# Performance work log

Measured on AMD Instinct MI355X. Metric: run time of the kernel, lower is better.

Reference implementation:

```python
import jax, jax.numpy as jnp
import numpy as np

R, N_X, N_MONTE = 8192, 32, 64


def setup_inputs() -> dict:
    key = jax.random.key(0)
    ks = jax.random.split(key, 6)
    # SPD per-step Hessian blocks (recog_x_prec_tilde is PSD by construction in the model)
    B = jax.random.normal(ks[0], (R, N_X, N_X), dtype=jnp.float32)
    x_hessian_diags = jnp.einsum('rij,rkj->rik', B, B) / N_X + jnp.eye(N_X, dtype=jnp.float32)
    x_grads = jax.random.normal(ks[1], (R, 1, N_X), dtype=jnp.float32)
    x_trans_mat = 0.5 * jnp.eye(N_X, dtype=jnp.float32) + 0.1 * jax.random.normal(ks[2], (N_X, N_X), dtype=jnp.float32)
    A = jax.random.normal(ks[3], (N_X, N_X), dtype=jnp.float32)
    x_trans_prec = A @ A.T / N_X + jnp.eye(N_X, dtype=jnp.float32)
    Bi = jax.random.normal(ks[4], (N_X, N_X), dtype=jnp.float32)
    x_init_prec = Bi @ Bi.T / N_X + jnp.eye(N_X, dtype=jnp.float32)
    epsx = jax.random.normal(ks[5], (R, N_MONTE, N_X), dtype=jnp.float32)
    return dict(x_hessian_diags=x_hessian_diags, x_grads=x_grads, x_trans_mat=x_trans_mat,
                x_trans_prec=x_trans_prec, x_init_prec=x_init_prec, epsx=epsx)


def _cholesky_update(x_hessian_diags, x_grads, x_trans_mat, x_trans_prec, x_init_prec, epsx):
    Rn, n_monte, n_x = epsx.shape
    solve = jax.scipy.linalg.solve_triangular
    MtP = x_trans_mat @ x_trans_prec          # [n_x, n_x]
    MtPMt = MtP @ x_trans_mat.T               # [n_x, n_x]
    # last step has no transition term (m=0), matching ms = [1,...,1,0]
    ms = jnp.concatenate([jnp.ones((Rn - 1,), jnp.float32), jnp.zeros((1,), jnp.float32)])

    def fwd(carry, elem):
        P, C, u = carry                       # predicted prec, off-diag chol, u
        H, g, m = elem
        L = jnp.linalg.cholesky(P + H + m * MtPMt)          # [n_x, n_x] lower
        u = solve(L, (g - u @ C.T).T, lower=True).T         # [1, n_x]
        C = solve(L, -MtP, lower=True).T                    # [n_x, n_x]
        P = x_trans_prec - C @ C.T
        return (P, C, u), (L, C, u)

    z = jnp.zeros((n_x, n_x), jnp.float32)
    init = (x_init_prec, z, jnp.zeros((1, n_x), jnp.float32))
    _, (Ls, Cs, us) = jax.lax.scan(fwd, init, (x_hessian_diags, x_grads, ms))

    gs = jnp.concatenate([us, epsx], axis=1)  # [R, 1+n_monte, n_x]

    def bwd(vw, elem):
        L, C, g = elem
        vw = solve(L.T, (g - vw @ C).T, lower=False).T      # [1+n_monte, n_x]
        return vw, vw

    _, vws = jax.lax.scan(bwd, jnp.zeros((n_monte + 1, n_x), jnp.float32),
                          (Ls, Cs, gs), reverse=True)
    vs, ws = vws[:, :1], vws[:, 1:]           # posterior mean part, sample part
    return Ls, Cs, vs, ws


def reference(x_hessian_diags, x_grads, x_trans_mat, x_trans_prec, x_init_prec, epsx):
    _, _, vs, ws = _cholesky_update(x_hessian_diags, x_grads, x_trans_mat,
                                    x_trans_prec, x_init_prec, epsx)
    # x_tilde = vs_tilde + ws_tilde as used downstream in _compute_eta_loss_2
    return vs + ws                            # [R, n_monte, n_x]
```

## Files before the change

### kernel.cpp

```cpp
#include <hip/hip_runtime.h>
#include <stdint.h>

#define RTOT 8192
#define BFWD 4
#define WFWD 12
#define BBWD 16
#define WBWD 16
#define LSTR 36

typedef unsigned short u16;
typedef __attribute__((ext_vector_type(4))) float f32x4;
typedef __attribute__((ext_vector_type(8))) unsigned short u16x8;

__device__ __forceinline__ float bf2f(u16 u) { return __uint_as_float(((uint32_t)u) << 16); }
__device__ __forceinline__ float rdlane(float v, int l) {
  return __int_as_float(__builtin_amdgcn_readlane(__float_as_int(v), l));
}

__device__ __forceinline__ void load8(const void* p, size_t off, bool bf, float* o) {
  if (bf) {
    u16x8 v = *(const u16x8*)((const u16*)p + off);
    #pragma unroll
    for (int e = 0; e < 8; ++e) o[e] = bf2f(v[e]);
  } else {
    f32x4 a = *(const f32x4*)((const float*)p + off);
    f32x4 b = *(const f32x4*)((const float*)p + off + 4);
    o[0]=a[0]; o[1]=a[1]; o[2]=a[2]; o[3]=a[3];
    o[4]=b[0]; o[5]=b[1]; o[6]=b[2]; o[7]=b[3];
  }
}
__device__ __forceinline__ float load1(const void* p, size_t off, bool bf) {
  return bf ? bf2f(((const u16*)p)[off]) : ((const float*)p)[off];
}

__global__ void detect_kernel(const void* Wptr, int* flag) {
  if (threadIdx.x == 0) {
    const u16* w = (const u16*)Wptr;
    int ok = 1;
    const int pi[4] = {0, 0, 1, 2};
    const int pj[4] = {1, 2, 2, 3};
    #pragma unroll
    for (int p = 0; p < 4; ++p)
      ok &= (w[pi[p]*32 + pj[p]] == w[pj[p]*32 + pi[p]]) ? 1 : 0;
    *flag = ok;
  }
}

__global__ __launch_bounds__(64, 2) void fwd_kernel(
    const void* __restrict__ Hg, const void* __restrict__ Gg,
    const void* __restrict__ Mg, const void* __restrict__ Wg,
    const void* __restrict__ Ig, int s0, const int* __restrict__ flag,
    float* __restrict__ gLinv, float* __restrict__ gCt, float* __restrict__ gU)
{
  __shared__ __align__(16) float ldsCt[32*LSTR];
  __shared__ __align__(16) float ldsLinv[32*LSTR];
  __shared__ float ldsU[32];

  const bool bf = (*flag != 0);
  const int lane = threadIdx.x & 63;
  const int il = lane & 31;
  const bool lo = (lane < 32);
  const int hoff = (lane >> 5) * 16;

  float wrow[32], mrow[32];
  #pragma unroll
  for (int c = 0; c < 4; ++c) {
    float wt[8], mt[8];
    load8(Wg, il*32 + c*8, bf, wt);
    load8(Mg, il*32 + c*8, bf, mt);
    #pragma unroll
    for (int e = 0; e < 8; ++e) {
      wrow[c*8+e] = wt[e]; mrow[c*8+e] = mt[e];
      ldsCt[il*LSTR + c*8+e] = mt[e];
    }
  }
  __syncthreads();

  #pragma unroll 4
  for (int m = 0; m < 32; ++m) {
    float acc = 0.0f;
    #pragma unroll
    for (int c = 0; c < 8; ++c) {
      f32x4 q = *(const f32x4*)&ldsCt[m*LSTR + c*4];
      acc = fmaf(q[0], wrow[c*4+0], acc); acc = fmaf(q[1], wrow[c*4+1], acc);
      acc = fmaf(q[2], wrow[c*4+2], acc); acc = fmaf(q[3], wrow[c*4+3], acc);
    }
    ldsLinv[m*LSTR + il] = acc;
  }
  __syncthreads();
  #pragma unroll 4
  for (int m = 0; m < 32; ++m) {
    float acc = 0.0f;
    #pragma unroll
    for (int c = 0; c < 8; ++c) {
      f32x4 q = *(const f32x4*)&ldsLinv[m*LSTR + c*4];
      acc = fmaf(q[0], mrow[c*4+0], acc); acc = fmaf(q[1], mrow[c*4+1], acc);
      acc = fmaf(q[2], mrow[c*4+2], acc); acc = fmaf(q[3], mrow[c*4+3], acc);
    }
    ldsCt[m*LSTR + il] = acc;
  }
  __syncthreads();

  float mtpcol[32];
  #pragma unroll
  for (int t = 0; t < 32; ++t) mtpcol[t] = ldsLinv[t*LSTR + il];
  float k0h[16];
  #pragma unroll
  for (int c = 0; c < 16; ++c) {
    float a = wrow[c]      + ldsCt[il*LSTR + c];
    float b = wrow[c + 16] + ldsCt[il*LSTR + 16 + c];
    k0h[c] = lo ? a : b;
  }
  __syncthreads();

  #pragma unroll
  for (int k = 0; k < 32; ++k) ldsCt[il*LSTR + k] = 0.0f;
  if (lo) ldsU[il] = 0.0f;
  __syncthreads();

  const int r0 = s0 + blockIdx.x * BFWD;
  const int rw0 = (r0 >= WFWD) ? (r0 - WFWD) : 0;
  const int rend = r0 + BFWD;

  float hcur[16];
  #pragma unroll
  for (int c = 0; c < 2; ++c)
    load8(Hg, (size_t)rw0*1024 + il*32 + hoff + c*8, bf, &hcur[c*8]);
  float gv = load1(Gg, (size_t)rw0*32 + il, bf);

  for (int r = rw0; r < rend; ++r) {
    int rn = (r + 1 < RTOT) ? (r + 1) : r;
    float hnext[16];
    #pragma unroll
    for (int c = 0; c < 2; ++c)
      load8(Hg, (size_t)rn*1024 + il*32 + hoff + c*8, bf, &hnext[c*8]);
    float gvn = load1(Gg, (size_t)rn*32 + il, bf);

    float sv[16];
    if (r == 0) {
      #pragma unroll
      for (int c = 0; c < 2; ++c) {
        float it[8], wt[8];
        load8(Ig, il*32 + hoff + c*8, bf, it);
        load8(Wg, il*32 + hoff + c*8, bf, wt);
        #pragma unroll
        for (int e = 0; e < 8; ++e)
          sv[c*8+e] = hcur[c*8+e] + it[e] + (k0h[c*8+e] - wt[e]);
      }
    } else if (r == RTOT - 1) {
      #pragma unroll
      for (int c = 0; c < 2; ++c) {
        float wt[8];
        load8(Wg, il*32 + hoff + c*8, bf, wt);
        #pragma unroll
        for (int e = 0; e < 8; ++e) sv[c*8+e] = hcur[c*8+e] + wt[e];
      }
    } else {
      #pragma unroll
      for (int k = 0; k < 16; ++k) sv[k] = hcur[k] + k0h[k];
    }

    float y = gv;
    #pragma unroll 4
    for (int m = 0; m < 32; ++m) {
      float cm = ldsCt[m*LSTR + il];
      y = fmaf(ldsU[m], cm, y);
      #pragma unroll
      for (int c = 0; c < 4; ++c) {
        f32x4 q = *(const f32x4*)&ldsCt[m*LSTR + hoff + c*4];
        sv[c*4+0] = fmaf(-cm, q[0], sv[c*4+0]);
        sv[c*4+1] = fmaf(-cm, q[1], sv[c*4+1]);
        sv[c*4+2] = fmaf(-cm, q[2], sv[c*4+2]);
        sv[c*4+3] = fmaf(-cm, q[3], sv[c*4+3]);
      }
    }

    float v[32];
    #pragma unroll
    for (int c = 0; c < 16; ++c) {
      float o = __shfl_xor(sv[c], 32, 64);
      v[c]      = lo ? sv[c] : mtpcol[c];
      v[c + 16] = lo ? o     : mtpcol[c + 16];
    }

    float un = 0.0f;
    float yr = y;
    if (r < r0) {
      #pragma unroll
      for (int j = 0; j < 32; ++j) {
        float dj = fmaxf(rdlane(v[j], j), 1e-12f);
        float rs = __builtin_amdgcn_rsqf(dj);
        float a = v[j] * rs;
        v[j] = a;
        float uj = rdlane(yr, j) * rs;
        yr = fmaf(-a, uj, yr);
        if (il == j) un = uj;
        #pragma unroll
        for (int k = j + 1; k < 32; ++k) {
          float bk = rdlane(v[j], k);
          v[k] = fmaf(-a, bk, v[k]);
        }
      }
    } else {
      float w[32];
      #pragma unroll
      for (int i = 0; i < 32; ++i) w[i] = (lo && il == i) ? 1.0f : 0.0f;
      #pragma unroll
      for (int j = 0; j < 32; ++j) {
        float dj = fmaxf(rdlane(v[j], j), 1e-12f);
        float rs = __builtin_amdgcn_rsqf(dj);
        float a = v[j] * rs;
        v[j] = a;
        float b = w[j] * rs;
        w[j] = b;
        float uj = rdlane(yr, j) * rs;
        yr = fmaf(-a, uj, yr);
        if (il == j) un = uj;
        #pragma unroll
        for (int k = j + 1; k < 32; ++k) {
          float bk = rdlane(v[j], k);
          v[k] = fmaf(-a, bk, v[k]);
          w[k] = fmaf(-b, bk, w[k]);
        }
      }
      if (lo) {
        #pragma unroll
        for (int i = 0; i < 32; ++i) ldsLinv[i*LSTR + il] = w[i];
      }
    }

    if (!lo) {
      #pragma unroll
      for (int m = 0; m < 32; ++m) ldsCt[m*LSTR + il] = v[m];
    } else {
      ldsU[il] = un;
    }

    if (r >= r0) {
      __syncthreads();
      size_t ro = (size_t)(r - s0);
      #pragma unroll
      for (int c = 0; c < 4; ++c) {
        int f = lane*16 + c*4;
        int mm = f >> 5, kk = f & 31;
        *(f32x4*)&gLinv[ro*1024 + f] = *(const f32x4*)&ldsLinv[mm*LSTR + kk];
        *(f32x4*)&gCt [ro*1024 + f] = *(const f32x4*)&ldsCt [mm*LSTR + kk];
      }
      if (lo) gU[ro*32 + il] = un;
    }

    #pragma unroll
    for (int e = 0; e < 16; ++e) hcur[e] = hnext[e];
    gv = gvn;
  }
}

__global__ __launch_bounds__(256, 2) void mid_kernel(
    const void* __restrict__ Eg, const int* __restrict__ flag,
    float* __restrict__ gLinv, float* __restrict__ gCt,
    float* __restrict__ gU, float* __restrict__ gY2, int s0)
{
  __shared__ __align__(16) float Li[32*LSTR];
  __shared__ __align__(16) float Ct_[32*LSTR];
  __shared__ float Ut[32];

  const bool bf = (*flag != 0);
  const int t = threadIdx.x;
  const size_t ro = blockIdx.x;
  const size_t r = (size_t)s0 + ro;

  {
    int mm = t >> 3, kk = (t & 7) * 4;
    *(f32x4*)&Li[mm*LSTR + kk]  = *(const f32x4*)&gLinv[ro*1024 + t*4];
    *(f32x4*)&Ct_[mm*LSTR + kk] = *(const f32x4*)&gCt [ro*1024 + t*4];
    if (t < 32) Ut[t] = gU[ro*32 + t];
  }
  __syncthreads();

  {
    int s = t >> 2, oct = t & 3;
    float er[32];
    #pragma unroll
    for (int c = 0; c < 4; ++c) load8(Eg, (r*64 + (size_t)s)*32 + c*8, bf, &er[c*8]);
    float a0=0,a1=0,a2=0,a3=0,a4=0,a5=0,a6=0,a7=0;
    #pragma unroll 4
    for (int k = 0; k < 32; ++k) {
      f32x4 b  = *(const f32x4*)&Li[k*LSTR + oct*8];
      f32x4 b2 = *(const f32x4*)&Li[k*LSTR + oct*8 + 4];
      float ek = er[k];
      a0=fmaf(ek,b[0],a0);  a1=fmaf(ek,b[1],a1);
      a2=fmaf(ek,b[2],a2);  a3=fmaf(ek,b[3],a3);
      a4=fmaf(ek,b2[0],a4); a5=fmaf(ek,b2[1],a5);
      a6=fmaf(ek,b2[2],a6); a7=fmaf(ek,b2[3],a7);
    }
    float* dst = (s < 32) ? (gLinv + ro*1024 + (size_t)s*32)
                          : (gY2  + ro*1024 + (size_t)(s-32)*32);
    f32x4 va = {a0,a1,a2,a3}, vb = {a4,a5,a6,a7};
    *(f32x4*)&dst[oct*8] = va;
    *(f32x4*)&dst[oct*8 + 4] = vb;
  }

  {
    int m = t >> 3, jo = t & 7;
    float d0=0,d1=0,d2=0,d3=0;
    #pragma unroll 4
    for (int k = 0; k < 32; ++k) {
      float cv = Ct_[k*LSTR + m];
      f32x4 b = *(const f32x4*)&Li[k*LSTR + jo*4];
      d0=fmaf(cv,b[0],d0); d1=fmaf(cv,b[1],d1);
      d2=fmaf(cv,b[2],d2); d3=fmaf(cv,b[3],d3);
    }
    f32x4 dv = {d0,d1,d2,d3};
    *(f32x4*)&gCt[ro*1024 + (size_t)m*32 + jo*4] = dv;
  }

  if (t < 32) {
    float a = 0.0f;
    #pragma unroll
    for (int k = 0; k < 32; ++k) a = fmaf(Ut[k], Li[k*LSTR + t], a);
    gU[ro*32 + t] = a;
  }
}

__global__ __launch_bounds__(256, 2) void bwd_kernel(
    const float* __restrict__ gD,
    const float* __restrict__ gY1,
    const float* __restrict__ gY2,
    const float* __restrict__ gY0,
    float* __restrict__ outg, int s0)
{
  __shared__ __align__(16) float vw[65*LSTR];
  __shared__ __align__(16) float Dl[2][32*LSTR];
  __shared__ __align__(16) float v0buf[2][32];

  const int t = threadIdx.x;
  const int pr = t >> 3;
  const int o  = t & 7;
  const int rowA = pr, rowB = pr + 32;
  const bool x64 = (t < 8);
  const int r0 = s0 + blockIdx.x * BBWD;
  int re = r0 + BBWD - 1 + WBWD; if (re > RTOT - 1) re = RTOT - 1;

  for (int i = t; i < 65*LSTR; i += 256) vw[i] = 0.0f;

  #define YPTR(RO_, S_) \
    ((S_) == 0  ? (gY0 + (size_t)(RO_)*32) : \
     (S_) <= 32 ? (gY1 + (size_t)(RO_)*1024 + (size_t)((S_)-1)*32) \
                : (gY2 + (size_t)(RO_)*1024 + (size_t)((S_)-33)*32))

  f32x4 z = {0,0,0,0};
  const int reo = re - s0;
  f32x4 pD = *(const f32x4*)&gD[(size_t)reo*1024 + t*4];
  f32x4 yA, yB, yC = z;
  yA = *(const f32x4*)&(YPTR(reo, rowA))[o*4];
  yB = *(const f32x4*)&(YPTR(reo, rowB))[o*4];
  if (x64) yC = *(const f32x4*)&(YPTR(reo, 64))[o*4];
  *(f32x4*)&Dl[re & 1][pr*LSTR + o*4] = pD;
  if (re > r0) pD = *(const f32x4*)&gD[(size_t)(reo-1)*1024 + t*4];
  __syncthreads();

  for (int r = re; r >= r0; --r) {
    const int cur = r & 1;
    const int ro = r - s0;

    if (r > r0) *(f32x4*)&Dl[cur ^ 1][pr*LSTR + o*4] = pD;
    f32x4 nyA = z, nyB = z, nyC = z;
    if (r - 1 > r0) pD = *(const f32x4*)&gD[(size_t)(ro-2)*1024 + t*4];
    if (r > r0) {
      nyA = *(const f32x4*)&(YPTR(ro - 1, rowA))[o*4];
      nyB = *(const f32x4*)&(YPTR(ro - 1, rowB))[o*4];
      if (x64) nyC = *(const f32x4*)&(YPTR(ro - 1, 64))[o*4];
    }

    float vrA[32], vrB[32];
    #pragma unroll
    for (int c = 0; c < 8; ++c) {
      f32x4 qa = *(const f32x4*)&vw[rowA*LSTR + c*4];
      f32x4 qb = *(const f32x4*)&vw[rowB*LSTR + c*4];
      vrA[c*4+0]=qa[0]; vrA[c*4+1]=qa[1]; vrA[c*4+2]=qa[2]; vrA[c*4+3]=qa[3];
      vrB[c*4+0]=qb[0]; vrB[c*4+1]=qb[1]; vrB[c*4+2]=qb[2]; vrB[c*4+3]=qb[3];
    }

    float a0=yA[0],a1=yA[1],a2=yA[2],a3=yA[3];
    float b0=yB[0],b1=yB[1],b2=yB[2],b3=yB[3];
    #pragma unroll 4
    for (int k = 0; k < 32; ++k) {
      f32x4 d = *(const f32x4*)&Dl[cur][k*LSTR + o*4];
      float xa = vrA[k], xb = vrB[k];
      a0=fmaf(xa,d[0],a0); a1=fmaf(xa,d[1],a1);
      a2=fmaf(xa,d[2],a2); a3=fmaf(xa,d[3],a3);
      b0=fmaf(xb,d[0],b0); b1=fmaf(xb,d[1],b1);
      b2=fmaf(xb,d[2],b2); b3=fmaf(xb,d[3],b3);
    }
    f32x4 va = {a0,a1,a2,a3}, vb = {b0,b1,b2,b3};
    *(f32x4*)&vw[rowA*LSTR + o*4] = va;
    *(f32x4*)&vw[rowB*LSTR + o*4] = vb;

    float c0=0,c1=0,c2=0,c3=0;
    if (x64) {
      *(f32x4*)&v0buf[cur][o*4] = va;
      float vrC[32];
      #pragma unroll
      for (int c = 0; c < 8; ++c) {
        f32x4 q = *(const f32x4*)&vw[64*LSTR + c*4];
        vrC[c*4+0]=q[0]; vrC[c*4+1]=q[1]; vrC[c*4+2]=q[2]; vrC[c*4+3]=q[3];
      }
      c0=yC[0]; c1=yC[1]; c2=yC[2]; c3=yC[3];
      #pragma unroll 4
      for (int k = 0; k < 32; ++k) {
        f32x4 d = *(const f32x4*)&Dl[cur][k*LSTR + o*4];
        float xc = vrC[k];
        c0=fmaf(xc,d[0],c0); c1=fmaf(xc,d[1],c1);
        c2=fmaf(xc,d[2],c2); c3=fmaf(xc,d[3],c3);
      }
      f32x4 vc = {c0,c1,c2,c3};
      *(f32x4*)&vw[64*LSTR + o*4] = vc;
    }

    __syncthreads();

    if (r < r0 + BBWD) {
      f32x4 v0 = *(const f32x4*)&v0buf[cur][o*4];
      if (pr >= 1) {
        float* dst = outg + ((size_t)r*64 + (size_t)(pr-1))*32 + o*4;
        f32x4 oo = {a0+v0[0], a1+v0[1], a2+v0[2], a3+v0[3]};
        *(f32x4*)dst = oo;
      }
      {
        float* dst = outg + ((size_t)r*64 + (size_t)(pr+31))*32 + o*4;
        f32x4 oo = {b0+v0[0], b1+v0[1], b2+v0[2], b3+v0[3]};
        *(f32x4*)dst = oo;
      }
      if (x64) {
        float* dst = outg + ((size_t)r*64 + 63)*32 + o*4;
        f32x4 oo = {c0+v0[0], c1+v0[1], c2+v0[2], c3+v0[3]};
        *(f32x4*)dst = oo;
      }
    }

    yA = nyA; yB = nyB;
    if (x64) yC = nyC;
  }
  #undef YPTR
}

extern "C" void kernel_launch(void* const* d_in, const int* in_sizes, int n_in,
                              void* d_out, int out_size, void* d_ws, size_t ws_size,
                              hipStream_t stream) {
  (void)in_sizes; (void)n_in; (void)out_size;
  const void* H = d_in[0];
  const void* G = d_in[1];
  const void* M = d_in[2];
  const void* W = d_in[3];
  const void* I = d_in[4];
  const void* E = d_in[5];
  float* out = (float*)d_out;

  int* flag = (int*)d_ws;
  float* ws0 = (float*)((char*)d_ws + 256);
  size_t avail = (ws_size > 256) ? (ws_size - 256) : 0;

  int nseg = 64;
  for (int cand = 1; cand <= 64; cand <<= 1) {
    size_t nrext = (size_t)(RTOT / cand) + WBWD;
    if (nrext * 12416 <= avail) { nseg = cand; break; }
  }
  const int segrows = RTOT / nseg;
  const size_t nrext_max = (size_t)segrows + WBWD;

  float* gLinv = ws0;
  float* gCt  = ws0 + nrext_max * 1024;
  float* gU   = ws0 + nrext_max * 2048;
  float* gY2  = ws0 + nrext_max * 2080;

  detect_kernel<<<1, 64, 0, stream>>>(W, flag);

  for (int s = 0; s < nseg; ++s) {
    int s0 = s * segrows;
    int s1ext = s0 + segrows + WBWD; if (s1ext > RTOT) s1ext = RTOT;
    int nr = s1ext - s0;
    int nfb = (nr + BFWD - 1) / BFWD;
    fwd_kernel<<<nfb, 64, 0, stream>>>(H, G, M, W, I, s0, flag, gLinv, gCt, gU);
    mid_kernel<<<nr, 256, 0, stream>>>(E, flag, gLinv, gCt, gU, gY2, s0);
    bwd_kernel<<<segrows / BBWD, 256, 0, stream>>>(gCt, gLinv, gY2, gU, out, s0);
  }
}
```

Before: 416.3 us.

## Fold mean term into sample rows and run backward scan in one wavefront

The mid kernel now adds the posterior-mean contribution (u·Linv) directly into every sample row's injected term. The mean row no longer has to be propagated separately, so the backward scan only tracks 64 rows. The backward kernel is rewritten as a single 64-lane wavefront that keeps each row's state in registers and broadcasts the D matrix via readlane. This removes LDS traffic and __syncthreads from the serial recurrence, and the backward block size is halved to raise the number of blocks. The cost is 32×32 readlane-fed FMAs per lane per step, plus more redundant warm-up steps relative to useful rows.

```diff
diff --git a/kernel.cpp b/kernel.cpp
--- a/kernel.cpp
+++ b/kernel.cpp
@@ -4,7 +4,7 @@
 #define RTOT 8192
 #define BFWD 4
 #define WFWD 12
-#define BBWD 16
+#define BBWD 8
 #define WBWD 16
 #define LSTR 36
 
@@ -258,11 +258,12 @@
 __global__ __launch_bounds__(256, 2) void mid_kernel(
     const void* __restrict__ Eg, const int* __restrict__ flag,
     float* __restrict__ gLinv, float* __restrict__ gCt,
-    float* __restrict__ gU, float* __restrict__ gY2, int s0)
+    const float* __restrict__ gU, float* __restrict__ gY2, int s0)
 {
   __shared__ __align__(16) float Li[32*LSTR];
   __shared__ __align__(16) float Ct_[32*LSTR];
   __shared__ float Ut[32];
+  __shared__ float Y0l[32];
 
   const bool bf = (*flag != 0);
   const int t = threadIdx.x;
@@ -274,6 +275,14 @@
     *(f32x4*)&Li[mm*LSTR + kk]  = *(const f32x4*)&gLinv[ro*1024 + t*4];
     *(f32x4*)&Ct_[mm*LSTR + kk] = *(const f32x4*)&gCt [ro*1024 + t*4];
     if (t < 32) Ut[t] = gU[ro*32 + t];
+  }
+  __syncthreads();
+
+  if (t < 32) {
+    float a = 0.0f;
+    #pragma unroll
+    for (int k = 0; k < 32; ++k) a = fmaf(Ut[k], Li[k*LSTR + t], a);
+    Y0l[t] = a;
   }
   __syncthreads();
 
@@ -293,9 +302,12 @@
       a4=fmaf(ek,b2[0],a4); a5=fmaf(ek,b2[1],a5);
       a6=fmaf(ek,b2[2],a6); a7=fmaf(ek,b2[3],a7);
     }
+    f32x4 y0a = *(const f32x4*)&Y0l[oct*8];
+    f32x4 y0b = *(const f32x4*)&Y0l[oct*8 + 4];
     float* dst = (s < 32) ? (gLinv + ro*1024 + (size_t)s*32)
                           : (gY2  + ro*1024 + (size_t)(s-32)*32);
-    f32x4 va = {a0,a1,a2,a3}, vb = {a4,a5,a6,a7};
+    f32x4 va = {a0+y0a[0], a1+y0a[1], a2+y0a[2], a3+y0a[3]};
+    f32x4 vb = {a4+y0b[0], a5+y0b[1], a6+y0b[2], a7+y0b[3]};
     *(f32x4*)&dst[oct*8] = va;
     *(f32x4*)&dst[oct*8 + 4] = vb;
   }
@@ -313,135 +325,80 @@
     f32x4 dv = {d0,d1,d2,d3};
     *(f32x4*)&gCt[ro*1024 + (size_t)m*32 + jo*4] = dv;
   }
-
-  if (t < 32) {
-    float a = 0.0f;
-    #pragma unroll
-    for (int k = 0; k < 32; ++k) a = fmaf(Ut[k], Li[k*LSTR + t], a);
-    gU[ro*32 + t] = a;
-  }
-}
-
-__global__ __launch_bounds__(256, 2) void bwd_kernel(
+}
+
+__global__ __launch_bounds__(64, 1) void bwd_kernel(
     const float* __restrict__ gD,
     const float* __restrict__ gY1,
     const float* __restrict__ gY2,
-    const float* __restrict__ gY0,
     float* __restrict__ outg, int s0)
 {
-  __shared__ __align__(16) float vw[65*LSTR];
-  __shared__ __align__(16) float Dl[2][32*LSTR];
-  __shared__ __align__(16) float v0buf[2][32];
-
-  const int t = threadIdx.x;
-  const int pr = t >> 3;
-  const int o  = t & 7;
-  const int rowA = pr, rowB = pr + 32;
-  const bool x64 = (t < 8);
+  const int l = threadIdx.x & 63;
+  const int lr = l & 31;
+  const int dco = (l >> 5) * 16;
   const int r0 = s0 + blockIdx.x * BBWD;
   int re = r0 + BBWD - 1 + WBWD; if (re > RTOT - 1) re = RTOT - 1;
 
-  for (int i = t; i < 65*LSTR; i += 256) vw[i] = 0.0f;
-
-  #define YPTR(RO_, S_) \
-    ((S_) == 0  ? (gY0 + (size_t)(RO_)*32) : \
-     (S_) <= 32 ? (gY1 + (size_t)(RO_)*1024 + (size_t)((S_)-1)*32) \
-                : (gY2 + (size_t)(RO_)*1024 + (size_t)((S_)-33)*32))
-
-  f32x4 z = {0,0,0,0};
+  const float* Yb = (l < 32) ? gY1 : gY2;
+
+  float vwr[32];
+  #pragma unroll
+  for (int k = 0; k < 32; ++k) vwr[k] = 0.0f;
+
   const int reo = re - s0;
-  f32x4 pD = *(const f32x4*)&gD[(size_t)reo*1024 + t*4];
-  f32x4 yA, yB, yC = z;
-  yA = *(const f32x4*)&(YPTR(reo, rowA))[o*4];
-  yB = *(const f32x4*)&(YPTR(reo, rowB))[o*4];
-  if (x64) yC = *(const f32x4*)&(YPTR(reo, 64))[o*4];
-  *(f32x4*)&Dl[re & 1][pr*LSTR + o*4] = pD;
-  if (re > r0) pD = *(const f32x4*)&gD[(size_t)(reo-1)*1024 + t*4];
-  __syncthreads();
+  f32x4 Dc[4], Yc[8];
+  #pragma unroll
+  for (int c = 0; c < 4; ++c)
+    Dc[c] = *(const f32x4*)&gD[(size_t)reo*1024 + (size_t)lr*32 + dco + c*4];
+  #pragma unroll
+  for (int c = 0; c < 8; ++c)
+    Yc[c] = *(const f32x4*)&Yb[(size_t)reo*1024 + (size_t)lr*32 + c*4];
 
   for (int r = re; r >= r0; --r) {
-    const int cur = r & 1;
     const int ro = r - s0;
 
-    if (r > r0) *(f32x4*)&Dl[cur ^ 1][pr*LSTR + o*4] = pD;
-    f32x4 nyA = z, nyB = z, nyC = z;
-    if (r - 1 > r0) pD = *(const f32x4*)&gD[(size_t)(ro-2)*1024 + t*4];
+    f32x4 Dn[4], Yn[8];
     if (r > r0) {
-      nyA = *(const f32x4*)&(YPTR(ro - 1, rowA))[o*4];
-      nyB = *(const f32x4*)&(YPTR(ro - 1, rowB))[o*4];
-      if (x64) nyC = *(const f32x4*)&(YPTR(ro - 1, 64))[o*4];
-    }
-
-    float vrA[32], vrB[32];
-    #pragma unroll
-    for (int c = 0; c < 8; ++c) {
-      f32x4 qa = *(const f32x4*)&vw[rowA*LSTR + c*4];
-      f32x4 qb = *(const f32x4*)&vw[rowB*LSTR + c*4];
-      vrA[c*4+0]=qa[0]; vrA[c*4+1]=qa[1]; vrA[c*4+2]=qa[2]; vrA[c*4+3]=qa[3];
-      vrB[c*4+0]=qb[0]; vrB[c*4+1]=qb[1]; vrB[c*4+2]=qb[2]; vrB[c*4+3]=qb[3];
-    }
-
-    float a0=yA[0],a1=yA[1],a2=yA[2],a3=yA[3];
-    float b0=yB[0],b1=yB[1],b2=yB[2],b3=yB[3];
-    #pragma unroll 4
-    for (int k = 0; k < 32; ++k) {
-      f32x4 d = *(const f32x4*)&Dl[cur][k*LSTR + o*4];
-      float xa = vrA[k], xb = vrB[k];
-      a0=fmaf(xa,d[0],a0); a1=fmaf(xa,d[1],a1);
-      a2=fmaf(xa,d[2],a2); a3=fmaf(xa,d[3],a3);
-      b0=fmaf(xb,d[0],b0); b1=fmaf(xb,d[1],b1);
-      b2=fmaf(xb,d[2],b2); b3=fmaf(xb,d[3],b3);
-    }
-    f32x4 va = {a0,a1,a2,a3}, vb = {b0,b1,b2,b3};
-    *(f32x4*)&vw[rowA*LSTR + o*4] = va;
-    *(f32x4*)&vw[rowB*LSTR + o*4] = vb;
-
-    float c0=0,c1=0,c2=0,c3=0;
-    if (x64) {
-      *(f32x4*)&v0buf[cur][o*4] = va;
-      float vrC[32];
+      #pragma unroll
+      for (int c = 0; c < 4; ++c)
+        Dn[c] = *(const f32x4*)&gD[(size_t)(ro-1)*1024 + (size_t)lr*32 + dco + c*4];
+      #pragma unroll
+      for (int c = 0; c < 8; ++c)
+        Yn[c] = *(const f32x4*)&Yb[(size_t)(ro-1)*1024 + (size_t)lr*32 + c*4];
+    }
+
+    float nv[32];
+    #pragma unroll
+    for (int j = 0; j < 32; ++j) {
+      float acc = Yc[j >> 2][j & 3];
+      const int cidx = j & 15;
+      const int sadd = (j >> 4) << 5;
+      #pragma unroll
+      for (int k = 0; k < 32; ++k) {
+        float dkj = rdlane(Dc[cidx >> 2][cidx & 3], k + sadd);
+        acc = fmaf(vwr[k], dkj, acc);
+      }
+      nv[j] = acc;
+    }
+
+    if (r < r0 + BBWD) {
+      float* dst = outg + ((size_t)r * 64 + (size_t)l) * 32;
       #pragma unroll
       for (int c = 0; c < 8; ++c) {
-        f32x4 q = *(const f32x4*)&vw[64*LSTR + c*4];
-        vrC[c*4+0]=q[0]; vrC[c*4+1]=q[1]; vrC[c*4+2]=q[2]; vrC[c*4+3]=q[3];
-      }
-      c0=yC[0]; c1=yC[1]; c2=yC[2]; c3=yC[3];
-      #pragma unroll 4
-      for (int k = 0; k < 32; ++k) {
-        f32x4 d = *(const f32x4*)&Dl[cur][k*LSTR + o*4];
-        float xc = vrC[k];
-        c0=fmaf(xc,d[0],c0); c1=fmaf(xc,d[1],c1);
-        c2=fmaf(xc,d[2],c2); c3=fmaf(xc,d[3],c3);
-      }
-      f32x4 vc = {c0,c1,c2,c3};
-      *(f32x4*)&vw[64*LSTR + o*4] = vc;
-    }
-
-    __syncthreads();
-
-    if (r < r0 + BBWD) {
-      f32x4 v0 = *(const f32x4*)&v0buf[cur][o*4];
-      if (pr >= 1) {
-        float* dst = outg + ((size_t)r*64 + (size_t)(pr-1))*32 + o*4;
-        f32x4 oo = {a0+v0[0], a1+v0[1], a2+v0[2], a3+v0[3]};
-        *(f32x4*)dst = oo;
-      }
-      {
-        float* dst = outg + ((size_t)r*64 + (size_t)(pr+31))*32 + o*4;
-        f32x4 oo = {b0+v0[0], b1+v0[1], b2+v0[2], b3+v0[3]};
-        *(f32x4*)dst = oo;
-      }
-      if (x64) {
-        float* dst = outg + ((size_t)r*64 + 63)*32 + o*4;
-        f32x4 oo = {c0+v0[0], c1+v0[1], c2+v0[2], c3+v0[3]};
-        *(f32x4*)dst = oo;
-      }
-    }
-
-    yA = nyA; yB = nyB;
-    if (x64) yC = nyC;
-  }
-  #undef YPTR
+        f32x4 o = { nv[c*4+0], nv[c*4+1], nv[c*4+2], nv[c*4+3] };
+        *(f32x4*)&dst[c*4] = o;
+      }
+    }
+
+    #pragma unroll
+    for (int k = 0; k < 32; ++k) vwr[k] = nv[k];
+    if (r > r0) {
+      #pragma unroll
+      for (int c = 0; c < 4; ++c) Dc[c] = Dn[c];
+      #pragma unroll
+      for (int c = 0; c < 8; ++c) Yc[c] = Yn[c];
+    }
+  }
 }
 
 extern "C" void kernel_launch(void* const* d_in, const int* in_sizes, int n_in,
@@ -482,6 +439,6 @@
     int nfb = (nr + BFWD - 1) / BFWD;
     fwd_kernel<<<nfb, 64, 0, stream>>>(H, G, M, W, I, s0, flag, gLinv, gCt, gU);
     mid_kernel<<<nr, 256, 0, stream>>>(E, flag, gLinv, gCt, gU, gY2, s0);
-    bwd_kernel<<<segrows / BBWD, 256, 0, stream>>>(gCt, gLinv, gY2, gU, out, s0);
-  }
-}
+    bwd_kernel<<<segrows / BBWD, 64, 0, stream>>>(gCt, gLinv, gY2, out, s0);
+  }
+}
```

Measured after the change: 483.6 us. 16.2% more time.
